# Kernel tuning notes

Measured on AMD Instinct MI355X. Metric: run time of the kernel, lower is better.

The kernel has to match this reference:

```python
import jax, jax.numpy as jnp
import numpy as np

B, COND_LEN, E = 128, 256, 512   # batch, cond_len, hidden_dim (== conditioning_dim)
A, L, H = 128, 64, 8             # action_dim, num_action_steps, num_heads
STEPS = 20
HD = E // H


def setup_inputs() -> dict:
    key = jax.random.key(0)
    ks = jax.random.split(key, 16)
    def rn(k, shape, s=0.02):
        return jax.random.normal(k, shape, jnp.float32) * s
    return {
        "conditioning": jax.random.normal(ks[0], (B, COND_LEN, E), jnp.float32),
        "noise": jax.random.normal(ks[1], (B, L, A), jnp.float32),
        # time_embed: Linear(1,E) -> ReLU -> Linear(E,E)
        "t1_w": rn(ks[2], (E, 1)), "t1_b": jnp.zeros((E,), jnp.float32),
        "t2_w": rn(ks[3], (E, E)), "t2_b": jnp.zeros((E,), jnp.float32),
        # query_proj: Linear(A, E)
        "qp_w": rn(ks[4], (E, A)), "qp_b": jnp.zeros((E,), jnp.float32),
        # MultiheadAttention packed in_proj (3E, E) and out_proj (E, E)
        "in_w": rn(ks[5], (3 * E, E)), "in_b": jnp.zeros((3 * E,), jnp.float32),
        "op_w": rn(ks[6], (E, E)), "op_b": jnp.zeros((E,), jnp.float32),
        # output_proj: Linear(E, A)
        "outp_w": rn(ks[7], (A, E)), "outp_b": jnp.zeros((A,), jnp.float32),
        # ffn: Linear(A, 4A) -> ReLU -> Linear(4A, A)
        "f1_w": rn(ks[8], (4 * A, A)), "f1_b": jnp.zeros((4 * A,), jnp.float32),
        "f2_w": rn(ks[9], (A, 4 * A)), "f2_b": jnp.zeros((A,), jnp.float32),
        # LayerNorm(A)
        "ln_g": jnp.ones((A,), jnp.float32), "ln_b": jnp.zeros((A,), jnp.float32),
    }


def reference(conditioning, noise, t1_w, t1_b, t2_w, t2_b, qp_w, qp_b,
              in_w, in_b, op_w, op_b, outp_w, outp_b,
              f1_w, f1_b, f2_w, f2_b, ln_g, ln_b):
    dt = -1.0 / STEPS
    scale = 1.0 / np.sqrt(HD)
    # K/V of cross-attn depend only on conditioning -> hoist out of the loop
    # (same math as recomputing per step).
    k = (conditioning @ in_w[E:2 * E].T + in_b[E:2 * E]).reshape(B, COND_LEN, H, HD)
    v = (conditioning @ in_w[2 * E:].T + in_b[2 * E:]).reshape(B, COND_LEN, H, HD)

    def denoise(x_t, time):
        t = time[:, None]                                            # (B,1)
        t_emb = jnp.maximum(t @ t1_w.T + t1_b, 0.0) @ t2_w.T + t2_b  # (B,E)
        q_in = x_t @ qp_w.T + qp_b + t_emb[:, None, :]               # (B,L,E)
        q = (q_in @ in_w[:E].T + in_b[:E]).reshape(B, L, H, HD)
        scores = jnp.einsum('bqhd,bkhd->bhqk', q * scale, k)         # (B,H,L,COND_LEN)
        attn = jax.nn.softmax(scores, axis=-1)
        ctx = jnp.einsum('bhqk,bkhd->bqhd', attn, v).reshape(B, L, E)
        ctx = ctx @ op_w.T + op_b                                    # MHA out_proj
        v_t = ctx @ outp_w.T + outp_b                                # (B,L,A)
        h = x_t + v_t
        mu = jnp.mean(h, axis=-1, keepdims=True)
        var = jnp.mean((h - mu) ** 2, axis=-1, keepdims=True)
        hn = (h - mu) / jnp.sqrt(var + 1e-5) * ln_g + ln_b
        return hn + (jnp.maximum(hn @ f1_w.T + f1_b, 0.0) @ f2_w.T + f2_b)

    def step(carry, _):
        x_t, time = carry
        v_t = denoise(x_t, time)
        return (x_t + dt * v_t, time + dt), None

    init = (noise, jnp.ones((B,), jnp.float32))
    (x_t, _), _ = jax.lax.scan(step, init, None, length=STEPS)
    return x_t
```

## Files before the change

### kernel.cpp

```cpp
#include <hip/hip_runtime.h>

#define NB 128
#define CL 256
#define EE 512
#define AA 128
#define LL 64
#define HH 8
#define HD 64
#define NSTEPS 20
#define BLROWS (NB*LL)
#define LOG2E 1.4426950408889634f
#define QSCALE 64.0f
#define INV_QS 0.015625f

typedef __attribute__((ext_vector_type(8))) short bf16x8;
typedef __attribute__((ext_vector_type(4))) float f32x4;
typedef unsigned int u32;

union F8 { u32 u[2]; long l; };

__device__ __forceinline__ unsigned short f2bf(float f) {
    union { float f; unsigned u; } x; x.f = f;
    unsigned u = x.u;
    u += 0x7fffu + ((u >> 16) & 1u);
    return (unsigned short)(u >> 16);
}
__device__ __forceinline__ u32 pk4f8(f32x4 v) {
    u32 r = __builtin_amdgcn_cvt_pk_fp8_f32(v[0], v[1], 0, false);
    r = __builtin_amdgcn_cvt_pk_fp8_f32(v[2], v[3], r, true);
    return r;
}
__device__ __forceinline__ unsigned char f2f8(float v) {
    return (unsigned char)(__builtin_amdgcn_cvt_pk_fp8_f32(v, v, 0, false) & 0xffu);
}

__device__ __forceinline__ void async_copy16(const unsigned short* g, unsigned short* l) {
    __builtin_amdgcn_global_load_lds((const __attribute__((address_space(1))) u32*)g,
                                     (__attribute__((address_space(3))) u32*)l, 16, 0, 0);
}

#define MFMA(a,b,c)  __builtin_amdgcn_mfma_f32_16x16x32_bf16(a, b, c, 0, 0, 0)
#define MFMA8(a,b,c) __builtin_amdgcn_mfma_f32_16x16x32_fp8_fp8(a, b, c, 0, 0, 0)

__device__ __forceinline__ F8 build8(const u32* p, int kk, int srcA, int srcB, int odd) {
    u32 a0 = __shfl((int)p[2*kk],   srcA, 64);
    u32 b0 = __shfl((int)p[2*kk+1], srcA, 64);
    u32 a1 = __shfl((int)p[2*kk],   srcB, 64);
    u32 b1 = __shfl((int)p[2*kk+1], srcB, 64);
    F8 f; f.u[0] = odd ? b0 : a0; f.u[1] = odd ? b1 : a1;
    return f;
}


__global__ void cvt8_kernel(const float* __restrict__ src, unsigned short* __restrict__ dst, int n8) {
    int i = blockIdx.x*256 + threadIdx.x;
    if (i >= n8) return;
    const float* s = src + (size_t)i*8;
    f32x4 v0 = *(const f32x4*)s;
    f32x4 v1 = *(const f32x4*)(s + 4);
    bf16x8 o;
    o[0]=(short)f2bf(v0[0]); o[1]=(short)f2bf(v0[1]);
    o[2]=(short)f2bf(v0[2]); o[3]=(short)f2bf(v0[3]);
    o[4]=(short)f2bf(v1[0]); o[5]=(short)f2bf(v1[1]);
    o[6]=(short)f2bf(v1[2]); o[7]=(short)f2bf(v1[3]);
    *(bf16x8*)(dst + (size_t)i*8) = o;
}

__global__ void prep_eff_kernel(const float* __restrict__ in_w, const float* __restrict__ qp_w,
                                const float* __restrict__ outp_w, const float* __restrict__ op_w,
                                const float* __restrict__ op_b, const float* __restrict__ outp_b,
                                unsigned short* __restrict__ wq, unsigned short* __restrict__ wo,
                                float* __restrict__ bo) {
    int tid = blockIdx.x*256 + threadIdx.x;
    if (tid < 65536) {
        int n = tid >> 7, k = tid & 127;
        float s = 0.f;
        for (int e = 0; e < 512; ++e) s += in_w[(size_t)n*512 + e] * qp_w[(size_t)e*128 + k];
        wq[(size_t)n*128 + k] = f2bf(s * (0.125f * LOG2E * QSCALE));
    } else if (tid < 131072) {
        int t2 = tid - 65536; int n = t2 >> 9, k = t2 & 511;
        float s = 0.f;
        for (int e = 0; e < 512; ++e) s += outp_w[(size_t)n*512 + e] * op_w[(size_t)e*512 + k];
        wo[(size_t)n*512 + k] = f2bf(s);
    } else if (tid < 131200) {
        int n = tid - 131072;
        float s = outp_b[n];
        for (int e = 0; e < 512; ++e) s += outp_w[(size_t)n*512 + e] * op_b[e];
        bo[n] = s;
    }
}

__global__ void temb_kernel(const float* __restrict__ t1_w, const float* __restrict__ t1_b,
                            const float* __restrict__ t2_w, const float* __restrict__ t2_b,
                            float* __restrict__ temb) {
    int tid = blockIdx.x*256 + threadIdx.x;
    if (tid >= NSTEPS*512) return;
    int s = tid >> 9, e = tid & 511;
    float t = 1.0f - 0.05f * (float)s;
    float acc = t2_b[e];
    for (int i = 0; i < 512; ++i)
        acc += t2_w[(size_t)e*512 + i] * fmaxf(t * t1_w[i] + t1_b[i], 0.f);
    temb[tid] = acc;
}

__global__ void qbias_kernel(const float* __restrict__ in_w, const float* __restrict__ in_b,
                             const float* __restrict__ qp_b, const float* __restrict__ temb,
                             float* __restrict__ qbias) {
    int tid = blockIdx.x*256 + threadIdx.x;
    if (tid >= NSTEPS*512) return;
    int s = tid >> 9, n = tid & 511;
    float acc = in_b[n];
    const float* te = temb + (size_t)s*512;
    for (int e = 0; e < 512; ++e)
        acc += in_w[(size_t)n*512 + e] * (qp_b[e] + te[e]);
    qbias[tid] = acc * (0.125f * LOG2E * QSCALE);
}

__global__ __launch_bounds__(512, 8) void kv_kernel(const unsigned short* __restrict__ condb,
                                                    const unsigned short* __restrict__ wkv,
                                                    const float* __restrict__ bias,
                                                    unsigned char* __restrict__ K8,
                                                    unsigned char* __restrict__ V8) {
    __shared__ unsigned short As[128*64];
    __shared__ unsigned short Bs[128*64];
    int tid = threadIdx.x;
    int blk = blockIdx.x;
    int xcd = blk & 7, j = blk >> 3;
    int m0 = (xcd*32 + (j >> 3)) * 128;
    int n0 = (j & 7) * 128;
    int wv = tid >> 6, lane = tid & 63, r = lane & 15, q = lane >> 4;
    int srow = lane >> 3;
    int sg = (lane & 7) ^ srow;
    const unsigned short* agl = condb + (size_t)(m0 + wv*16 + srow)*512 + sg*8;
    const unsigned short* bgl = wkv   + (size_t)(n0 + wv*16 + srow)*512 + sg*8;
    f32x4 acc[8] = {};
#pragma unroll
    for (int kt = 0; kt < 8; ++kt) {
        int k0 = kt * 64;
#pragma unroll
        for (int ii = 0; ii < 2; ++ii) {
            async_copy16(agl + (size_t)(ii*8)*512 + k0, &As[(wv*16 + ii*8)*64]);
            async_copy16(bgl + (size_t)(ii*8)*512 + k0, &Bs[(wv*16 + ii*8)*64]);
        }
        __syncthreads();
#pragma unroll
        for (int kk = 0; kk < 2; ++kk) {
            int gof = ((kk*4 + q) ^ (r & 7)) * 8;
            bf16x8 a = *(const bf16x8*)&As[(wv*16 + r)*64 + gof];
#pragma unroll
            for (int t = 0; t < 8; ++t) {
                bf16x8 b = *(const bf16x8*)&Bs[(t*16 + r)*64 + gof];
                acc[t] = MFMA(a, b, acc[t]);
            }
        }
        __syncthreads();
    }
    int mbase = m0 + wv*16 + q*4;
    int bb = mbase >> 8, kpb = mbase & 255;
#pragma unroll
    for (int t = 0; t < 8; ++t) {
        int n = n0 + t*16 + r;
        float bs = bias[n];
        if (n < 512) {
            int h = n >> 6, d = n & 63;
            int colp = ((d>>3)&3)*16 + ((d>>5)&1)*8 + (d&7);
            unsigned char* kp = K8 + (size_t)(bb*HH + h)*16384 + colp;
#pragma unroll
            for (int i = 0; i < 4; ++i)
                kp[(kpb + i)*64] = f2f8(acc[t][i] + bs);
        } else {
            int n2 = n - 512, h = n2 >> 6, d = n2 & 63;
            int kk = kpb >> 5, qq = (kpb >> 3) & 3, jb = kpb & 7;
            int colv = (kk>>1)*64 + qq*16 + (kk&1)*8 + jb;
            u32 w01 = __builtin_amdgcn_cvt_pk_fp8_f32(acc[t][0]+bs, acc[t][1]+bs, 0, false);
            w01 = __builtin_amdgcn_cvt_pk_fp8_f32(acc[t][2]+bs, acc[t][3]+bs, w01, true);
            *(u32*)(V8 + (size_t)(bb*HH + h)*16384 + d*256 + colv) = w01;
        }
    }
}

__global__ __launch_bounds__(512, 2) void mega_kernel(
        const unsigned char* __restrict__ Kg,
        const unsigned char* __restrict__ Vg,
        const float* __restrict__ noise,
        const unsigned short* __restrict__ wq,
        const float* __restrict__ qbiasB,
        const unsigned short* __restrict__ wo,
        const float* __restrict__ bo,
        const float* __restrict__ ln_g, const float* __restrict__ ln_b,
        const unsigned short* __restrict__ f1w,
        const float* __restrict__ f1_b,
        const unsigned short* __restrict__ f2w,
        const float* __restrict__ f2_b,
        float* __restrict__ outp) {
    __shared__ unsigned short xS[32*136];
    __shared__ unsigned short cuS[32*520];
    __shared__ unsigned short hnS[32*136];
    __shared__ float redS[32*4], redS2[32*4];

    int tid = threadIdx.x, w = tid >> 6, lane = tid & 63, r = lane & 15, q = lane >> 4;
    int vblk = ((blockIdx.x & 7) << 5) | (blockIdx.x >> 3);
    int b = vblk >> 1;
    int row0 = vblk * 32;
    int h = w;
    int tB = w & 1, cg = w >> 1;
    int srcA = r + ((2*q) & 3)*16;
    int srcB = r + ((2*q + 1) & 3)*16;
    int odd = (q >> 1) & 1;

    float xf[2][4];
#pragma unroll
    for (int t = 0; t < 2; ++t)
#pragma unroll
        for (int i = 0; i < 4; ++i) {
            int rl = tB*16 + q*4 + i, col = cg*32 + t*16 + r;
            float v = noise[(size_t)(row0 + rl)*AA + col];
            xf[t][i] = v;
            xS[rl*136 + col] = f2bf(v);
        }

    size_t bh = (size_t)b*HH + h;
    const unsigned char* kbase = Kg + bh*16384;
    const unsigned char* vbase = Vg + bh*16384;
    __syncthreads();

    const float dt = -1.f / (float)NSTEPS;

#pragma unroll 1
    for (int s = 0; s < NSTEPS; ++s) {
        const float* qb_s = qbiasB + (size_t)s*512;

        {
            f32x4 qacc0[4] = {}, qacc1[4] = {};
#pragma unroll
            for (int kk = 0; kk < 4; ++kk) {
                bf16x8 bx0 = *(const bf16x8*)&xS[(r)*136 + kk*32 + q*8];
                bf16x8 bx1 = *(const bf16x8*)&xS[(16 + r)*136 + kk*32 + q*8];
#pragma unroll
                for (int t = 0; t < 4; ++t) {
                    bf16x8 a = *(const bf16x8*)(wq + (size_t)(h*HD + t*16 + r)*AA + kk*32 + q*8);
                    qacc0[t] = MFMA(a, bx0, qacc0[t]);
                    qacc1[t] = MFMA(a, bx1, qacc1[t]);
                }
            }
            u32 qp0[4], qp1[4];
#pragma unroll
            for (int t = 0; t < 4; ++t) {
                f32x4 qb4 = *(const f32x4*)(qb_s + h*HD + t*16 + q*4);
                f32x4 v0, v1;
#pragma unroll
                for (int i = 0; i < 4; ++i) { v0[i] = qacc0[t][i] + qb4[i]; v1[i] = qacc1[t][i] + qb4[i]; }
                qp0[t] = pk4f8(v0);
                qp1[t] = pk4f8(v1);
            }
            F8 bq0[2], bq1[2];
            bq0[0] = build8(qp0, 0, srcA, srcB, odd);
            bq0[1] = build8(qp0, 1, srcA, srcB, odd);
            bq1[0] = build8(qp1, 0, srcA, srcB, odd);
            bq1[1] = build8(qp1, 1, srcA, srcB, odd);

            float m0r = -3e38f, m1r = -3e38f;
            float l0 = 0.f, l1 = 0.f;
            f32x4 c0[4] = {}, c1[4] = {};

#pragma unroll
            for (int hh = 0; hh < 2; ++hh) {
                uint4 kbuf[8];
#pragma unroll
                for (int t = 0; t < 8; ++t)
                    kbuf[t] = *(const uint4*)(kbase + (size_t)((hh*8 + t)*16 + r)*64 + q*16);

                f32x4 s0[8] = {}, s1[8] = {};
#pragma unroll
                for (int t = 0; t < 8; ++t) {
                    F8 k0, k1;
                    k0.u[0] = kbuf[t].x; k0.u[1] = kbuf[t].y;
                    k1.u[0] = kbuf[t].z; k1.u[1] = kbuf[t].w;
                    s0[t] = MFMA8(k0.l, bq0[0].l, s0[t]);
                    s0[t] = MFMA8(k1.l, bq0[1].l, s0[t]);
                    s1[t] = MFMA8(k0.l, bq1[0].l, s1[t]);
                    s1[t] = MFMA8(k1.l, bq1[1].l, s1[t]);
                }

                uint4 vbuf[8];
#pragma unroll
                for (int kp = 0; kp < 2; ++kp)
#pragma unroll
                    for (int t = 0; t < 4; ++t)
                        vbuf[kp*4 + t] = *(const uint4*)(vbase + (size_t)(t*16 + r)*256 + (hh*2 + kp)*64 + q*16);

                float a0 = s0[0][0], a1 = s0[0][1], a2 = s0[0][2], a3 = s0[0][3];
                float b0 = s1[0][0], b1 = s1[0][1], b2 = s1[0][2], b3 = s1[0][3];
#pragma unroll
                for (int t = 1; t < 8; ++t) {
                    a0 = fmaxf(a0, s0[t][0]); a1 = fmaxf(a1, s0[t][1]);
                    a2 = fmaxf(a2, s0[t][2]); a3 = fmaxf(a3, s0[t][3]);
                    b0 = fmaxf(b0, s1[t][0]); b1 = fmaxf(b1, s1[t][1]);
                    b2 = fmaxf(b2, s1[t][2]); b3 = fmaxf(b3, s1[t][3]);
                }
                float hm0 = fmaxf(fmaxf(a0, a1), fmaxf(a2, a3));
                float hm1 = fmaxf(fmaxf(b0, b1), fmaxf(b2, b3));
                hm0 = fmaxf(hm0, __shfl_xor(hm0, 16));
                hm0 = fmaxf(hm0, __shfl_xor(hm0, 32));
                hm1 = fmaxf(hm1, __shfl_xor(hm1, 16));
                hm1 = fmaxf(hm1, __shfl_xor(hm1, 32));
                float nm0 = fmaxf(m0r, hm0 * INV_QS);
                float nm1 = fmaxf(m1r, hm1 * INV_QS);
                float rs0 = exp2f(m0r - nm0);
                float rs1 = exp2f(m1r - nm1);
                m0r = nm0; m1r = nm1;

                u32 pp0[8], pp1[8];
                float t00 = 0.f, t01 = 0.f, t10 = 0.f, t11 = 0.f;
#pragma unroll
                for (int t = 0; t < 8; ++t) {
                    float e0 = exp2f(fmaf(s0[t][0], INV_QS, -nm0));
                    float e1 = exp2f(fmaf(s0[t][1], INV_QS, -nm0));
                    float e2 = exp2f(fmaf(s0[t][2], INV_QS, -nm0));
                    float e3 = exp2f(fmaf(s0[t][3], INV_QS, -nm0));
                    t00 += e0 + e2; t01 += e1 + e3;
                    f32x4 w0; w0[0]=e0*QSCALE; w0[1]=e1*QSCALE; w0[2]=e2*QSCALE; w0[3]=e3*QSCALE;
                    pp0[t] = pk4f8(w0);
                    float f0 = exp2f(fmaf(s1[t][0], INV_QS, -nm1));
                    float f1 = exp2f(fmaf(s1[t][1], INV_QS, -nm1));
                    float f2 = exp2f(fmaf(s1[t][2], INV_QS, -nm1));
                    float f3 = exp2f(fmaf(s1[t][3], INV_QS, -nm1));
                    t10 += f0 + f2; t11 += f1 + f3;
                    f32x4 w1; w1[0]=f0*QSCALE; w1[1]=f1*QSCALE; w1[2]=f2*QSCALE; w1[3]=f3*QSCALE;
                    pp1[t] = pk4f8(w1);
                }
                l0 = l0 * rs0 + (t00 + t01);
                l1 = l1 * rs1 + (t10 + t11);

                float rr0[4], rr1[4];
#pragma unroll
                for (int i = 0; i < 4; ++i) {
                    rr0[i] = __shfl(rs0, q*4 + i);
                    rr1[i] = __shfl(rs1, q*4 + i);
                }
#pragma unroll
                for (int t = 0; t < 4; ++t)
#pragma unroll
                    for (int i = 0; i < 4; ++i) {
                        c0[t][i] *= rr0[i];
                        c1[t][i] *= rr1[i];
                    }

#pragma unroll
                for (int kp = 0; kp < 2; ++kp) {
                    F8 a00 = build8(pp0, 2*kp,   srcA, srcB, odd);
                    F8 a01 = build8(pp0, 2*kp+1, srcA, srcB, odd);
                    F8 a10 = build8(pp1, 2*kp,   srcA, srcB, odd);
                    F8 a11 = build8(pp1, 2*kp+1, srcA, srcB, odd);
#pragma unroll
                    for (int t = 0; t < 4; ++t) {
                        F8 v0, v1;
                        v0.u[0] = vbuf[kp*4+t].x; v0.u[1] = vbuf[kp*4+t].y;
                        v1.u[0] = vbuf[kp*4+t].z; v1.u[1] = vbuf[kp*4+t].w;
                        c0[t] = MFMA8(a00.l, v0.l, c0[t]);
                        c0[t] = MFMA8(a01.l, v1.l, c0[t]);
                        c1[t] = MFMA8(a10.l, v0.l, c1[t]);
                        c1[t] = MFMA8(a11.l, v1.l, c1[t]);
                    }
                }
            }

            l0 += __shfl_xor(l0, 16); l0 += __shfl_xor(l0, 32);
            l1 += __shfl_xor(l1, 16); l1 += __shfl_xor(l1, 32);
            float iv0 = 1.0f / l0, iv1 = 1.0f / l1;
            float sc0[4], sc1[4];
#pragma unroll
            for (int i = 0; i < 4; ++i) {
                sc0[i] = INV_QS * __shfl(iv0, q*4 + i);
                sc1[i] = INV_QS * __shfl(iv1, q*4 + i);
            }
#pragma unroll
            for (int t = 0; t < 4; ++t)
#pragma unroll
                for (int i = 0; i < 4; ++i) {
                    cuS[(q*4 + i)*520 + h*HD + t*16 + r]      = f2bf(c0[t][i] * sc0[i]);
                    cuS[(16 + q*4 + i)*520 + h*HD + t*16 + r] = f2bf(c1[t][i] * sc1[i]);
                }
        }
        __syncthreads();

        f32x4 oacc[2] = {};
#pragma unroll
        for (int kk = 0; kk < 16; ++kk) {
            bf16x8 a = *(const bf16x8*)&cuS[(tB*16 + r)*520 + kk*32 + q*8];
#pragma unroll
            for (int t = 0; t < 2; ++t) {
                bf16x8 bw = *(const bf16x8*)(wo + (size_t)(cg*32 + t*16 + r)*EE + kk*32 + q*8);
                oacc[t] = MFMA(a, bw, oacc[t]);
            }
        }
        float hv[2][4];
#pragma unroll
        for (int t = 0; t < 2; ++t) {
            float bov = bo[cg*32 + t*16 + r];
#pragma unroll
            for (int i = 0; i < 4; ++i) hv[t][i] = oacc[t][i] + bov + xf[t][i];
        }
#pragma unroll
        for (int i = 0; i < 4; ++i) {
            float s1 = hv[0][i] + hv[1][i];
            float s2 = hv[0][i]*hv[0][i] + hv[1][i]*hv[1][i];
            s1 += __shfl_xor(s1, 1);  s2 += __shfl_xor(s2, 1);
            s1 += __shfl_xor(s1, 2);  s2 += __shfl_xor(s2, 2);
            s1 += __shfl_xor(s1, 4);  s2 += __shfl_xor(s2, 4);
            s1 += __shfl_xor(s1, 8);  s2 += __shfl_xor(s2, 8);
            if (r == 0) { redS[(tB*16 + q*4 + i)*4 + cg] = s1; redS2[(tB*16 + q*4 + i)*4 + cg] = s2; }
        }
        __syncthreads();
        float hnv[2][4];
#pragma unroll
        for (int i = 0; i < 4; ++i) {
            int row = tB*16 + q*4 + i;
            float s1 = redS [row*4+0] + redS [row*4+1] + redS [row*4+2] + redS [row*4+3];
            float s2 = redS2[row*4+0] + redS2[row*4+1] + redS2[row*4+2] + redS2[row*4+3];
            float mu = s1 * (1.f/128.f);
            float var = s2 * (1.f/128.f) - mu*mu;
            float rstd = rsqrtf(var + 1e-5f);
#pragma unroll
            for (int t = 0; t < 2; ++t) {
                int col = cg*32 + t*16 + r;
                float v = (hv[t][i] - mu) * rstd * ln_g[col] + ln_b[col];
                hnv[t][i] = v;
                hnS[row*136 + col] = f2bf(v);
            }
        }
        __syncthreads();

        f32x4 o2[2] = {};
#pragma unroll 1
        for (int nt = 0; nt < 4; ++nt) {
            f32x4 a1[2] = {};
#pragma unroll
            for (int kk = 0; kk < 4; ++kk) {
                bf16x8 a = *(const bf16x8*)&hnS[(tB*16 + r)*136 + kk*32 + q*8];
#pragma unroll
                for (int t = 0; t < 2; ++t) {
                    bf16x8 bw = *(const bf16x8*)(f1w + (size_t)(nt*128 + cg*32 + t*16 + r)*AA + kk*32 + q*8);
                    a1[t] = MFMA(a, bw, a1[t]);
                }
            }
#pragma unroll
            for (int t = 0; t < 2; ++t) {
                float b1 = f1_b[nt*128 + cg*32 + t*16 + r];
#pragma unroll
                for (int i = 0; i < 4; ++i)
                    cuS[(tB*16 + q*4 + i)*520 + nt*128 + cg*32 + t*16 + r] = f2bf(fmaxf(a1[t][i] + b1, 0.f));
            }
        }
        __syncthreads();
#pragma unroll 1
        for (int nt = 0; nt < 4; ++nt) {
#pragma unroll
            for (int kk = 0; kk < 4; ++kk) {
                bf16x8 a = *(const bf16x8*)&cuS[(tB*16 + r)*520 + nt*128 + kk*32 + q*8];
#pragma unroll
                for (int t = 0; t < 2; ++t) {
                    bf16x8 bw = *(const bf16x8*)(f2w + (size_t)(cg*32 + t*16 + r)*EE + nt*128 + kk*32 + q*8);
                    o2[t] = MFMA(a, bw, o2[t]);
                }
            }
        }

        if (s < NSTEPS - 1) {
#pragma unroll
            for (int t = 0; t < 2; ++t) {
                float b2 = f2_b[cg*32 + t*16 + r];
#pragma unroll
                for (int i = 0; i < 4; ++i) {
                    float outv = hnv[t][i] + o2[t][i] + b2;
                    float xn = xf[t][i] + dt * outv;
                    xf[t][i] = xn;
                    xS[(tB*16 + q*4 + i)*136 + cg*32 + t*16 + r] = f2bf(xn);
                }
            }
            __syncthreads();
        } else {
#pragma unroll
            for (int t = 0; t < 2; ++t) {
                float b2 = f2_b[cg*32 + t*16 + r];
#pragma unroll
                for (int i = 0; i < 4; ++i) {
                    float outv = hnv[t][i] + o2[t][i] + b2;
                    outp[(size_t)(row0 + tB*16 + q*4 + i)*AA + cg*32 + t*16 + r] = xf[t][i] + dt * outv;
                }
            }
        }
    }
}

extern "C" void kernel_launch(void* const* d_in, const int* in_sizes, int n_in,
                              void* d_out, int out_size, void* d_ws, size_t ws_size,
                              hipStream_t stream) {
    const float* cond   = (const float*)d_in[0];
    const float* noise  = (const float*)d_in[1];
    const float* t1_w   = (const float*)d_in[2];
    const float* t1_b   = (const float*)d_in[3];
    const float* t2_w   = (const float*)d_in[4];
    const float* t2_b   = (const float*)d_in[5];
    const float* qp_w   = (const float*)d_in[6];
    const float* qp_b   = (const float*)d_in[7];
    const float* in_w   = (const float*)d_in[8];
    const float* in_b   = (const float*)d_in[9];
    const float* op_w   = (const float*)d_in[10];
    const float* op_b   = (const float*)d_in[11];
    const float* outp_w = (const float*)d_in[12];
    const float* outp_b = (const float*)d_in[13];
    const float* f1_w   = (const float*)d_in[14];
    const float* f1_b   = (const float*)d_in[15];
    const float* f2_w   = (const float*)d_in[16];
    const float* f2_b   = (const float*)d_in[17];
    const float* ln_g   = (const float*)d_in[18];
    const float* ln_bp  = (const float*)d_in[19];

    char* w = (char*)d_ws;
    auto alloc = [&](size_t bytes) {
        char* p = w;
        w += (bytes + 255) & ~(size_t)255;
        return p;
    };
    unsigned char*  K8     = (unsigned char*)alloc((size_t)NB*HH*CL*HD);
    unsigned char*  V8     = (unsigned char*)alloc((size_t)NB*HH*HD*CL);
    unsigned short* condb  = (unsigned short*)alloc((size_t)NB*CL*EE*2);
    unsigned short* wkv_bf = (unsigned short*)alloc((size_t)1024*512*2);
    unsigned short* wq_bf  = (unsigned short*)alloc((size_t)512*128*2);
    unsigned short* wo_bf  = (unsigned short*)alloc((size_t)128*512*2);
    unsigned short* f1_bf  = (unsigned short*)alloc((size_t)512*128*2);
    unsigned short* f2_bf  = (unsigned short*)alloc((size_t)128*512*2);
    float*          bo_eff = (float*)alloc(128*4);
    float*          tembB  = (float*)alloc((size_t)NSTEPS*512*4);
    float*          qbiasB = (float*)alloc((size_t)NSTEPS*512*4);
    (void)ws_size; (void)n_in; (void)in_sizes; (void)out_size;

    cvt8_kernel<<<8192, 256, 0, stream>>>(cond, condb, NB*CL*EE/8);
    cvt8_kernel<<<256, 256, 0, stream>>>(in_w + 512*512, wkv_bf, 1024*512/8);
    cvt8_kernel<<<32, 256, 0, stream>>>(f1_w, f1_bf, 512*128/8);
    cvt8_kernel<<<32, 256, 0, stream>>>(f2_w, f2_bf, 128*512/8);
    prep_eff_kernel<<<513, 256, 0, stream>>>(in_w, qp_w, outp_w, op_w, op_b, outp_b,
                                             wq_bf, wo_bf, bo_eff);
    temb_kernel<<<40, 256, 0, stream>>>(t1_w, t1_b, t2_w, t2_b, tembB);
    qbias_kernel<<<40, 256, 0, stream>>>(in_w, in_b, qp_b, tembB, qbiasB);
    kv_kernel<<<2048, 512, 0, stream>>>(condb, wkv_bf, in_b + 512, K8, V8);

    mega_kernel<<<256, 512, 0, stream>>>(K8, V8, noise, wq_bf, qbiasB,
                                         wo_bf, bo_eff, ln_g, ln_bp,
                                         f1_bf, f1_b, f2_bf, f2_b,
                                         (float*)d_out);
}
```

Baseline: 1.312 ms.

## Halve mega_kernel block to 4 waves, each handling two heads and both row tiles

The fused denoising kernel now launches 256 threads per block instead of 512. Each wave loops over two attention heads and computes both 16-row tiles in the output projection, LayerNorm and FFN stages, so every weight fragment it loads feeds two MFMAs. This cuts redundant weight loads and halves the number of waves taking part in each block barrier. The cost is half as many waves per CU to hide latency, more serial work per wave and higher register pressure.

```diff
diff --git a/kernel.cpp b/kernel.cpp
--- a/kernel.cpp
+++ b/kernel.cpp
@@ -179,7 +179,7 @@
     }
 }
 
-__global__ __launch_bounds__(512, 2) void mega_kernel(
+__global__ __launch_bounds__(256, 1) void mega_kernel(
         const unsigned char* __restrict__ Kg,
         const unsigned char* __restrict__ Vg,
         const float* __restrict__ noise,
@@ -202,26 +202,22 @@
     int vblk = ((blockIdx.x & 7) << 5) | (blockIdx.x >> 3);
     int b = vblk >> 1;
     int row0 = vblk * 32;
-    int h = w;
-    int tB = w & 1, cg = w >> 1;
     int srcA = r + ((2*q) & 3)*16;
     int srcB = r + ((2*q + 1) & 3)*16;
     int odd = (q >> 1) & 1;
 
-    float xf[2][4];
-#pragma unroll
-    for (int t = 0; t < 2; ++t)
-#pragma unroll
-        for (int i = 0; i < 4; ++i) {
-            int rl = tB*16 + q*4 + i, col = cg*32 + t*16 + r;
-            float v = noise[(size_t)(row0 + rl)*AA + col];
-            xf[t][i] = v;
-            xS[rl*136 + col] = f2bf(v);
-        }
-
-    size_t bh = (size_t)b*HH + h;
-    const unsigned char* kbase = Kg + bh*16384;
-    const unsigned char* vbase = Vg + bh*16384;
+    float xf[2][2][4];
+#pragma unroll
+    for (int tile = 0; tile < 2; ++tile)
+#pragma unroll
+        for (int t = 0; t < 2; ++t)
+#pragma unroll
+            for (int i = 0; i < 4; ++i) {
+                int rl = tile*16 + q*4 + i, col = w*32 + t*16 + r;
+                float v = noise[(size_t)(row0 + rl)*AA + col];
+                xf[tile][t][i] = v;
+                xS[rl*136 + col] = f2bf(v);
+            }
     __syncthreads();
 
     const float dt = -1.f / (float)NSTEPS;
@@ -230,7 +226,12 @@
     for (int s = 0; s < NSTEPS; ++s) {
         const float* qb_s = qbiasB + (size_t)s*512;
 
-        {
+#pragma unroll 1
+        for (int hp = 0; hp < 2; ++hp) {
+            int h = w*2 + hp;
+            const unsigned char* kbase = Kg + ((size_t)b*HH + h)*16384;
+            const unsigned char* vbase = Vg + ((size_t)b*HH + h)*16384;
+
             f32x4 qacc0[4] = {}, qacc1[4] = {};
 #pragma unroll
             for (int kk = 0; kk < 4; ++kk) {
@@ -384,72 +385,89 @@
         }
         __syncthreads();
 
-        f32x4 oacc[2] = {};
+        f32x4 oacc[2][2] = {};
 #pragma unroll
         for (int kk = 0; kk < 16; ++kk) {
-            bf16x8 a = *(const bf16x8*)&cuS[(tB*16 + r)*520 + kk*32 + q*8];
+            bf16x8 aT0 = *(const bf16x8*)&cuS[(r)*520 + kk*32 + q*8];
+            bf16x8 aT1 = *(const bf16x8*)&cuS[(16 + r)*520 + kk*32 + q*8];
 #pragma unroll
             for (int t = 0; t < 2; ++t) {
-                bf16x8 bw = *(const bf16x8*)(wo + (size_t)(cg*32 + t*16 + r)*EE + kk*32 + q*8);
-                oacc[t] = MFMA(a, bw, oacc[t]);
-            }
-        }
-        float hv[2][4];
+                bf16x8 bw = *(const bf16x8*)(wo + (size_t)(w*32 + t*16 + r)*EE + kk*32 + q*8);
+                oacc[0][t] = MFMA(aT0, bw, oacc[0][t]);
+                oacc[1][t] = MFMA(aT1, bw, oacc[1][t]);
+            }
+        }
+        float hv[2][2][4];
 #pragma unroll
         for (int t = 0; t < 2; ++t) {
-            float bov = bo[cg*32 + t*16 + r];
-#pragma unroll
-            for (int i = 0; i < 4; ++i) hv[t][i] = oacc[t][i] + bov + xf[t][i];
-        }
-#pragma unroll
-        for (int i = 0; i < 4; ++i) {
-            float s1 = hv[0][i] + hv[1][i];
-            float s2 = hv[0][i]*hv[0][i] + hv[1][i]*hv[1][i];
-            s1 += __shfl_xor(s1, 1);  s2 += __shfl_xor(s2, 1);
-            s1 += __shfl_xor(s1, 2);  s2 += __shfl_xor(s2, 2);
-            s1 += __shfl_xor(s1, 4);  s2 += __shfl_xor(s2, 4);
-            s1 += __shfl_xor(s1, 8);  s2 += __shfl_xor(s2, 8);
-            if (r == 0) { redS[(tB*16 + q*4 + i)*4 + cg] = s1; redS2[(tB*16 + q*4 + i)*4 + cg] = s2; }
-        }
+            float bov = bo[w*32 + t*16 + r];
+#pragma unroll
+            for (int tile = 0; tile < 2; ++tile)
+#pragma unroll
+                for (int i = 0; i < 4; ++i)
+                    hv[tile][t][i] = oacc[tile][t][i] + bov + xf[tile][t][i];
+        }
+#pragma unroll
+        for (int tile = 0; tile < 2; ++tile)
+#pragma unroll
+            for (int i = 0; i < 4; ++i) {
+                float s1 = hv[tile][0][i] + hv[tile][1][i];
+                float s2 = hv[tile][0][i]*hv[tile][0][i] + hv[tile][1][i]*hv[tile][1][i];
+                s1 += __shfl_xor(s1, 1);  s2 += __shfl_xor(s2, 1);
+                s1 += __shfl_xor(s1, 2);  s2 += __shfl_xor(s2, 2);
+                s1 += __shfl_xor(s1, 4);  s2 += __shfl_xor(s2, 4);
+                s1 += __shfl_xor(s1, 8);  s2 += __shfl_xor(s2, 8);
+                if (r == 0) {
+                    redS [(tile*16 + q*4 + i)*4 + w] = s1;
+                    redS2[(tile*16 + q*4 + i)*4 + w] = s2;
+                }
+            }
         __syncthreads();
-        float hnv[2][4];
-#pragma unroll
-        for (int i = 0; i < 4; ++i) {
-            int row = tB*16 + q*4 + i;
-            float s1 = redS [row*4+0] + redS [row*4+1] + redS [row*4+2] + redS [row*4+3];
-            float s2 = redS2[row*4+0] + redS2[row*4+1] + redS2[row*4+2] + redS2[row*4+3];
-            float mu = s1 * (1.f/128.f);
-            float var = s2 * (1.f/128.f) - mu*mu;
-            float rstd = rsqrtf(var + 1e-5f);
-#pragma unroll
-            for (int t = 0; t < 2; ++t) {
-                int col = cg*32 + t*16 + r;
-                float v = (hv[t][i] - mu) * rstd * ln_g[col] + ln_b[col];
-                hnv[t][i] = v;
-                hnS[row*136 + col] = f2bf(v);
-            }
-        }
+        float hnv[2][2][4];
+#pragma unroll
+        for (int tile = 0; tile < 2; ++tile)
+#pragma unroll
+            for (int i = 0; i < 4; ++i) {
+                int row = tile*16 + q*4 + i;
+                float s1 = redS [row*4+0] + redS [row*4+1] + redS [row*4+2] + redS [row*4+3];
+                float s2 = redS2[row*4+0] + redS2[row*4+1] + redS2[row*4+2] + redS2[row*4+3];
+                float mu = s1 * (1.f/128.f);
+                float var = s2 * (1.f/128.f) - mu*mu;
+                float rstd = rsqrtf(var + 1e-5f);
+#pragma unroll
+                for (int t = 0; t < 2; ++t) {
+                    int col = w*32 + t*16 + r;
+                    float v = (hv[tile][t][i] - mu) * rstd * ln_g[col] + ln_b[col];
+                    hnv[tile][t][i] = v;
+                    hnS[row*136 + col] = f2bf(v);
+                }
+            }
         __syncthreads();
 
-        f32x4 o2[2] = {};
+        f32x4 o2[2][2] = {};
 #pragma unroll 1
         for (int nt = 0; nt < 4; ++nt) {
-            f32x4 a1[2] = {};
+            f32x4 a1[2][2] = {};
 #pragma unroll
             for (int kk = 0; kk < 4; ++kk) {
-                bf16x8 a = *(const bf16x8*)&hnS[(tB*16 + r)*136 + kk*32 + q*8];
+                bf16x8 aT0 = *(const bf16x8*)&hnS[(r)*136 + kk*32 + q*8];
+                bf16x8 aT1 = *(const bf16x8*)&hnS[(16 + r)*136 + kk*32 + q*8];
 #pragma unroll
                 for (int t = 0; t < 2; ++t) {
-                    bf16x8 bw = *(const bf16x8*)(f1w + (size_t)(nt*128 + cg*32 + t*16 + r)*AA + kk*32 + q*8);
-                    a1[t] = MFMA(a, bw, a1[t]);
+                    bf16x8 bw = *(const bf16x8*)(f1w + (size_t)(nt*128 + w*32 + t*16 + r)*AA + kk*32 + q*8);
+                    a1[0][t] = MFMA(aT0, bw, a1[0][t]);
+                    a1[1][t] = MFMA(aT1, bw, a1[1][t]);
                 }
             }
 #pragma unroll
             for (int t = 0; t < 2; ++t) {
-                float b1 = f1_b[nt*128 + cg*32 + t*16 + r];
-#pragma unroll
-                for (int i = 0; i < 4; ++i)
-                    cuS[(tB*16 + q*4 + i)*520 + nt*128 + cg*32 + t*16 + r] = f2bf(fmaxf(a1[t][i] + b1, 0.f));
+                float b1 = f1_b[nt*128 + w*32 + t*16 + r];
+#pragma unroll
+                for (int tile = 0; tile < 2; ++tile)
+#pragma unroll
+                    for (int i = 0; i < 4; ++i)
+                        cuS[(tile*16 + q*4 + i)*520 + nt*128 + w*32 + t*16 + r] =
+                            f2bf(fmaxf(a1[tile][t][i] + b1, 0.f));
             }
         }
         __syncthreads();
@@ -457,11 +475,13 @@
         for (int nt = 0; nt < 4; ++nt) {
 #pragma unroll
             for (int kk = 0; kk < 4; ++kk) {
-                bf16x8 a = *(const bf16x8*)&cuS[(tB*16 + r)*520 + nt*128 + kk*32 + q*8];
+                bf16x8 aT0 = *(const bf16x8*)&cuS[(r)*520 + nt*128 + kk*32 + q*8];
+                bf16x8 aT1 = *(const bf16x8*)&cuS[(16 + r)*520 + nt*128 + kk*32 + q*8];
 #pragma unroll
                 for (int t = 0; t < 2; ++t) {
-                    bf16x8 bw = *(const bf16x8*)(f2w + (size_t)(cg*32 + t*16 + r)*EE + nt*128 + kk*32 + q*8);
-                    o2[t] = MFMA(a, bw, o2[t]);
+                    bf16x8 bw = *(const bf16x8*)(f2w + (size_t)(w*32 + t*16 + r)*EE + nt*128 + kk*32 + q*8);
+                    o2[0][t] = MFMA(aT0, bw, o2[0][t]);
+                    o2[1][t] = MFMA(aT1, bw, o2[1][t]);
                 }
             }
         }
@@ -469,25 +489,30 @@
         if (s < NSTEPS - 1) {
 #pragma unroll
             for (int t = 0; t < 2; ++t) {
-                float b2 = f2_b[cg*32 + t*16 + r];
-#pragma unroll
-                for (int i = 0; i < 4; ++i) {
-                    float outv = hnv[t][i] + o2[t][i] + b2;
-                    float xn = xf[t][i] + dt * outv;
-                    xf[t][i] = xn;
-                    xS[(tB*16 + q*4 + i)*136 + cg*32 + t*16 + r] = f2bf(xn);
-                }
+                float b2 = f2_b[w*32 + t*16 + r];
+#pragma unroll
+                for (int tile = 0; tile < 2; ++tile)
+#pragma unroll
+                    for (int i = 0; i < 4; ++i) {
+                        float outv = hnv[tile][t][i] + o2[tile][t][i] + b2;
+                        float xn = xf[tile][t][i] + dt * outv;
+                        xf[tile][t][i] = xn;
+                        xS[(tile*16 + q*4 + i)*136 + w*32 + t*16 + r] = f2bf(xn);
+                    }
             }
             __syncthreads();
         } else {
 #pragma unroll
             for (int t = 0; t < 2; ++t) {
-                float b2 = f2_b[cg*32 + t*16 + r];
-#pragma unroll
-                for (int i = 0; i < 4; ++i) {
-                    float outv = hnv[t][i] + o2[t][i] + b2;
-                    outp[(size_t)(row0 + tB*16 + q*4 + i)*AA + cg*32 + t*16 + r] = xf[t][i] + dt * outv;
-                }
+                float b2 = f2_b[w*32 + t*16 + r];
+#pragma unroll
+                for (int tile = 0; tile < 2; ++tile)
+#pragma unroll
+                    for (int i = 0; i < 4; ++i) {
+                        float outv = hnv[tile][t][i] + o2[tile][t][i] + b2;
+                        outp[(size_t)(row0 + tile*16 + q*4 + i)*AA + w*32 + t*16 + r] =
+                            xf[tile][t][i] + dt * outv;
+                    }
             }
         }
     }
@@ -546,7 +571,7 @@
     qbias_kernel<<<40, 256, 0, stream>>>(in_w, in_b, qp_b, tembB, qbiasB);
     kv_kernel<<<2048, 512, 0, stream>>>(condb, wkv_bf, in_b + 512, K8, V8);
 
-    mega_kernel<<<256, 512, 0, stream>>>(K8, V8, noise, wq_bf, qbiasB,
+    mega_kernel<<<256, 256, 0, stream>>>(K8, V8, noise, wq_bf, qbiasB,
                                          wo_bf, bo_eff, ln_g, ln_bp,
                                          f1_bf, f1_b, f2_bf, f2_b,
                                          (float*)d_out);
```

Result: faster. 1.239 ms (-5.6%).
